# Kernel tuning notes

Measured on AMD Instinct MI355X. Metric: run time of the kernel, lower is better.

## Reference

```python
import math
import jax, jax.numpy as jnp
import numpy as np

B, T, E, H = 8, 2048, 512, 8
NQ_H, NL = 4, 2          # qubits per attention head, circuit layers
NQ_F, FFN = 8, 2048      # FFN qubits, ffn_dim

# ---- batched state-vector quantum simulation -------------------------------
# state shape: [N, 2, 2, ..., 2] (one axis of size 2 per qubit; wire q = axis q+1)

def apply_ry(state, q, theta):
    """RY(theta) on wire q. theta: scalar or [N] (per-batch angle)."""
    th = jnp.asarray(theta) * 0.5
    c, s = jnp.cos(th), jnp.sin(th)
    if th.ndim == 1:
        shp = (-1,) + (1,) * (state.ndim - 2)
        c, s = c.reshape(shp), s.reshape(shp)
    s0 = jax.lax.index_in_dim(state, 0, axis=q + 1, keepdims=False)
    s1 = jax.lax.index_in_dim(state, 1, axis=q + 1, keepdims=False)
    return jnp.stack([c * s0 - s * s1, s * s0 + c * s1], axis=q + 1)

def apply_cnot(state, ctrl, tgt):
    c0 = jax.lax.index_in_dim(state, 0, axis=ctrl + 1, keepdims=True)
    c1 = jax.lax.index_in_dim(state, 1, axis=ctrl + 1, keepdims=True)
    c1 = jnp.flip(c1, axis=tgt + 1)  # X on target when control = 1
    return jnp.concatenate([c0, c1], axis=ctrl + 1)

def run_circuit(x, params):
    """x: [N, n] data angles. params: [L, n] (shared) or [N, L, n] (per-element).
    Circuit: L x (RY(params) layer + CNOT chain + ring CNOT), then RY(x), then <Z_q>.
    Returns [N, n] PauliZ expectations."""
    N, n = x.shape
    L = params.shape[-2]
    state = jnp.zeros((N, 2 ** n), x.dtype).at[:, 0].set(1.0).reshape((N,) + (2,) * n)
    for l in range(L):
        for q in range(n):
            theta = params[:, l, q] if params.ndim == 3 else params[l, q]
            state = apply_ry(state, q, theta)
        for q in range(n - 1):
            state = apply_cnot(state, q, q + 1)
        state = apply_cnot(state, n - 1, 0)
    for q in range(n):
        state = apply_ry(state, q, x[:, q])
    probs = (state ** 2).reshape(N, 2 ** n)
    bits = (jnp.arange(2 ** n)[:, None] >> (n - 1 - jnp.arange(n))) & 1  # wire 0 = MSB
    return probs @ (1 - 2 * bits).astype(x.dtype)  # [N, n]

def layer_norm(x, g, b, eps=1e-5):
    m = x.mean(-1, keepdims=True)
    v = ((x - m) ** 2).mean(-1, keepdims=True)
    return (x - m) / jnp.sqrt(v + eps) * g + b

def setup_inputs() -> dict:
    key = jax.random.key(0)
    ks = jax.random.split(key, 9)
    def lin(k, o, i):
        return jax.random.normal(k, (o, i), jnp.float32) / np.sqrt(i).astype(np.float32)
    return {
        "x": jax.random.normal(ks[0], (B, T, E), jnp.float32),
        "wq": lin(ks[1], E, E), "wk": lin(ks[2], E, E),
        "wv": lin(ks[3], E, E), "wo": lin(ks[4], E, E),
        "head_params": jax.random.normal(ks[5], (H, NL, NQ_H), jnp.float32),
        "ffn_params": jax.random.normal(ks[6], (2, NQ_F), jnp.float32),
        "w1": lin(ks[7], FFN, NQ_F), "w2": lin(ks[8], E, FFN),
        "g1": jnp.ones((E,), jnp.float32), "b1": jnp.zeros((E,), jnp.float32),
        "g2": jnp.ones((E,), jnp.float32), "b2": jnp.zeros((E,), jnp.float32),
    }

def reference(x, wq, wk, wv, wo, head_params, ffn_params, w1, w2, g1, b1, g2, b2):
    Bb, Tt, Ee = x.shape
    hd = Ee // H
    BT = Bb * Tt
    # ---- quantum multi-head attention (dropout = eval/identity) ----
    q = x @ wq.T; k = x @ wk.T; v = x @ wv.T
    scores = jnp.einsum('bte,bse->bts', q, k) / math.sqrt(Ee)  # NOTE: scale by sqrt(E)
    attn = jax.nn.softmax(scores, axis=-1)
    out = jnp.einsum('bts,bse->bte', attn, v)                  # [B,T,E]
    oh = out.reshape(Bb, Tt, H, hd)
    # fold heads into the batch dim; per-head params broadcast per element
    xh = oh[..., :NQ_H].transpose(2, 0, 1, 3).reshape(H * BT, NQ_H)
    ph = jnp.broadcast_to(head_params[:, None], (H, BT, NL, NQ_H)).reshape(H * BT, NL, NQ_H)
    qout = run_circuit(xh, ph)                                  # [H*BT, NQ_H]
    qout = jnp.pad(qout, ((0, 0), (0, hd - NQ_H)))              # zero-pad to head_dim
    qout = qout.reshape(H, Bb, Tt, hd).transpose(1, 2, 0, 3).reshape(Bb, Tt, Ee)
    attn_out = qout @ wo.T
    x1 = layer_norm(x + attn_out, g1, b1)
    # ---- quantum FFN (only ffn_params[0] used, as in source) ----
    xf = x1.reshape(BT, Ee)[:, :NQ_F]
    f = run_circuit(xf, ffn_params[:1]).reshape(Bb, Tt, NQ_F)
    f = jax.nn.relu(f @ w1.T) @ w2.T
    return layer_norm(x1 + f, g2, b2)
```

## Files before the change

kernel.cpp:

```cpp
#include <hip/hip_runtime.h>
#include <hip/hip_bf16.h>
#include <math.h>


#define B_   8
#define T_   2048
#define E_   512

typedef __attribute__((ext_vector_type(8))) short bf16x8;
typedef __attribute__((ext_vector_type(4))) short bf16x4;
typedef __attribute__((ext_vector_type(4))) float f32x4;

#define GLL16(g, l) __builtin_amdgcn_global_load_lds((const __attribute__((address_space(1))) void*)(g), (__attribute__((address_space(3))) void*)(l), 16, 0, 0)

__device__ inline unsigned short f2bf(float f){
  union { float f; unsigned u; } v; v.f = f;
  unsigned r = v.u + 0x7fff + ((v.u >> 16) & 1);
  return (unsigned short)(r >> 16);
}

__global__ __launch_bounds__(256) void k0_setup(const float* __restrict__ hp,
                         const float* __restrict__ fp,
                         const float* __restrict__ wo, float* __restrict__ cAB,
                         unsigned short* __restrict__ wo32b) {
  int t = threadIdx.x, bi = blockIdx.x;
  if (bi > 0) {
    int gid = (bi-1)*256 + t;
    int e = gid >> 3, c4 = gid & 7;
    float4 v = *(const float4*)(wo + (size_t)e*512 + c4*64);
    unsigned short h[4] = { f2bf(v.x), f2bf(v.y), f2bf(v.z), f2bf(v.w) };
    *(unsigned long long*)(wo32b + (size_t)e*32 + c4*4) = *(unsigned long long*)h;
    return;
  }
  __shared__ float fst[256], tmp[256], ra[256], rb[256];
  fst[t] = (t == 0) ? 1.f : 0.f;
  __syncthreads();
  #pragma unroll
  for (int q = 0; q < 8; ++q) {
    int str = 1 << (7-q);
    float th = 0.5f * fp[q];
    float c = cosf(th), s = sinf(th);
    float self = fst[t], part = fst[t ^ str];
    float nv = (t & str) ? (c*self + s*part) : (c*self - s*part);
    __syncthreads();
    tmp[t] = nv;
    __syncthreads();
    fst[t] = tmp[t];
    __syncthreads();
  }
  #pragma unroll
  for (int g = 0; g < 8; ++g) {
    int ctrl = (g < 7) ? g : 7, tgt = (g < 7) ? g+1 : 0;
    int cs = 1 << (7-ctrl), tsr = 1 << (7-tgt);
    float nv = fst[(t & cs) ? (t ^ tsr) : t];
    __syncthreads();
    fst[t] = nv;
    __syncthreads();
  }
  #pragma unroll
  for (int q = 0; q < 8; ++q) {
    int str = 1 << (7-q);
    float a = fst[t]*fst[t] * ((t & str) ? -1.f : 1.f);
    float b = fst[t]*fst[t ^ str];
    ra[t] = a; rb[t] = b;
    __syncthreads();
    for (int off = 128; off > 0; off >>= 1){
      if (t < off){ ra[t] += ra[t+off]; rb[t] += rb[t+off]; }
      __syncthreads();
    }
    if (t == 0){ cAB[64+q] = ra[0]; cAB[72+q] = rb[0]; }
    __syncthreads();
  }
  if (t < 8) {
    float st[16];
    #pragma unroll
    for (int i=0;i<16;i++) st[i]=0.f;
    st[0]=1.f;
    for (int l=0;l<2;l++){
      for (int q=0;q<4;q++){
        float th = 0.5f*hp[t*8 + l*4 + q];
        float c = cosf(th), s = sinf(th);
        int str = 1<<(3-q);
        for (int i=0;i<16;i++) if (!(i & str)) {
          float s0=st[i], s1=st[i|str];
          st[i]     = c*s0 - s*s1;
          st[i|str] = s*s0 + c*s1;
        }
      }
      for (int q=0;q<4;q++){
        int ctrl = (q<3)? q : 3, tgt = (q<3)? q+1 : 0;
        int cs = 1<<(3-ctrl), tsr = 1<<(3-tgt);
        for (int i=0;i<16;i++) if ((i&cs) && !(i&tsr)) {
          float tt = st[i]; st[i]=st[i|tsr]; st[i|tsr]=tt;
        }
      }
    }
    for (int q=0;q<4;q++){
      int str = 1<<(3-q);
      float A=0.f, Bv=0.f;
      for (int i=0;i<16;i++){
        A  += st[i]*st[i] * ((i&str)? -1.f : 1.f);
        Bv += st[i]*st[i^str];
      }
      cAB[t*4+q]    = A;
      cAB[32+t*4+q] = Bv;
    }
  }
}

__global__ __launch_bounds__(256) void kc_cast(const float* __restrict__ x,
                     const float* __restrict__ wq, const float* __restrict__ wk,
                     const float* __restrict__ w2, unsigned short* __restrict__ xb,
                     unsigned short* __restrict__ wqkb, unsigned short* __restrict__ w2b){
  int bi = blockIdx.x;
  if (bi < 4096) {
    int i = bi*256 + threadIdx.x;
    const float4* p = (const float4*)x + (size_t)i*2;
    float4 a = p[0], b = p[1];
    union { unsigned short h[8]; uint4 u; } o;
    o.h[0]=f2bf(a.x); o.h[1]=f2bf(a.y); o.h[2]=f2bf(a.z); o.h[3]=f2bf(a.w);
    o.h[4]=f2bf(b.x); o.h[5]=f2bf(b.y); o.h[6]=f2bf(b.z); o.h[7]=f2bf(b.w);
    ((uint4*)xb)[i] = o.u;
    return;
  }
  int i = (bi-4096)*256 + threadIdx.x;
  const float* src; unsigned short* dst; float s = 1.f;
  if (i < 65536){
    int row = i >> 6, c8 = (i & 63)*8;
    if (row < 512){ src = wq + (size_t)row*512 + c8; s = 0.044194173824159216f; }
    else          { src = wk + (size_t)(row-512)*512 + c8; }
    dst = wqkb + (size_t)row*512 + c8;
  } else {
    int j = i - 65536;
    src = w2 + (size_t)j*8; dst = w2b + (size_t)j*8;
  }
  float4 a = *(const float4*)src, b = *(const float4*)(src+4);
  union { unsigned short h[8]; uint4 u; } o;
  o.h[0]=f2bf(a.x*s); o.h[1]=f2bf(a.y*s); o.h[2]=f2bf(a.z*s); o.h[3]=f2bf(a.w*s);
  o.h[4]=f2bf(b.x*s); o.h[5]=f2bf(b.y*s); o.h[6]=f2bf(b.z*s); o.h[7]=f2bf(b.w*s);
  *(uint4*)dst = o.u;
}

template<int K, int LDC, bool OUTBF, int GX, int GM>
__global__ __launch_bounds__(256,2) void gemm_bt(
    const unsigned short* __restrict__ A, const unsigned short* __restrict__ Bw,
    void* __restrict__ C, int m_base){
  __shared__ __align__(16) char sm[16384];
  char* As = sm; char* Bs = sm + 8192;
  int t = threadIdx.x, w = t>>6, l = t&63;
  int lr = l&15, quad = l>>4;
  int lin = blockIdx.x;
  int n0 = ((lin >> 3) % GX) * 128;
  int m0 = ((lin & 7) * (GM/8) + lin / (8*GX)) * 128;
  int wr = (w>>1)*64, wc = (w&1)*64;
  f32x4 acc[4][4] = {};
  for (int k0 = 0; k0 < K; k0 += 32){
    __syncthreads();
    #pragma unroll
    for (int c = 0; c < 2; ++c){
      int ch = c*256 + t, row = ch>>2, sw = ch&3, lc = sw ^ ((row>>1)&3);
      GLL16(A  + (size_t)(m0+row)*K + k0 + lc*8, As + c*4096 + w*1024);
      GLL16(Bw + (size_t)(n0+row)*K + k0 + lc*8, Bs + c*4096 + w*1024);
    }
    __syncthreads();
    bf16x8 af[4], bg[4];
    #pragma unroll
    for (int i=0;i<4;++i){
      int ra = wr + i*16 + lr;
      af[i] = *(const bf16x8*)(As + ra*64 + (quad ^ ((ra>>1)&3))*16);
      int rb = wc + i*16 + lr;
      bg[i] = *(const bf16x8*)(Bs + rb*64 + (quad ^ ((rb>>1)&3))*16);
    }
    #pragma unroll
    for (int i=0;i<4;++i)
      #pragma unroll
      for (int j=0;j<4;++j)
        acc[i][j] = __builtin_amdgcn_mfma_f32_16x16x32_bf16(af[i], bg[j], acc[i][j], 0,0,0);
  }
  #pragma unroll
  for (int i=0;i<4;++i)
    #pragma unroll
    for (int j=0;j<4;++j)
      #pragma unroll
      for (int r=0;r<4;++r){
        size_t row = (size_t)(m_base + m0 + wr + i*16 + quad*4 + r);
        int col = n0 + wc + j*16 + lr;
        if constexpr (OUTBF) ((unsigned short*)C)[row*LDC + col] = f2bf(acc[i][j][r]);
        else                 ((float*)C)[row*LDC + col] = acc[i][j][r];
      }
}

__global__ __launch_bounds__(256) void k1_v32(const float* __restrict__ x,
    const float* __restrict__ wv, unsigned short* __restrict__ v32t) {
  int m0 = blockIdx.x * 64;
  __shared__ float Xs[64][36];
  __shared__ float Ws[32][36];
  int t = threadIdx.x;
  int m = t >> 2, c0 = (t & 3) * 8;
  float acc[8] = {};
  for (int k0 = 0; k0 < 512; k0 += 32) {
    #pragma unroll
    for (int u=0; u<2; u++){
      int idx = t + u*256;
      int r = idx >> 3, c4 = (idx & 7) * 4;
      *(float4*)&Xs[r][c4] = *(const float4*)(x + (size_t)(m0+r)*512 + k0 + c4);
    }
    { int r = t >> 3, c4 = (t & 7) * 4;
      int wrow = (r>>2)*64 + (r&3);
      *(float4*)&Ws[r][c4] = *(const float4*)(wv + (size_t)wrow*512 + k0 + c4);
    }
    __syncthreads();
    #pragma unroll
    for (int kk=0; kk<32; kk++){
      float xv = Xs[m][kk];
      #pragma unroll
      for (int j=0;j<8;j++) acc[j] += xv * Ws[c0+j][kk];
    }
    __syncthreads();
  }
  int tok = m0 + m, bb = tok >> 11, s = tok & 2047;
  #pragma unroll
  for (int j=0;j<8;j++)
    v32t[((size_t)(bb*32 + c0 + j))*2048 + s] = f2bf(acc[j]);
}

__global__ __launch_bounds__(256,1) void k2_attn(
    const unsigned short* __restrict__ qkb, const unsigned short* __restrict__ v32t,
    float* __restrict__ Opart, float* __restrict__ mlb){
  __shared__ __align__(16) char sm[57856];
  char* Qc  = sm;
  char* Ks  = sm + 8192;
  char* Vts = sm + 40960;
  float* OtL = (float*)sm;
  float* mL  = (float*)(sm + 36864);
  float* lL  = (float*)(sm + 37888);

  int t = threadIdx.x, w = t>>6, l = t&63;
  int lr = l & 15, quad = l >> 4;
  int lin = blockIdx.x;
  int b = lin & 7;
  int m0 = ((lin >> 3) & 31) * 64;
  int half = lin >> 8;
  size_t bT = (size_t)b*2048;
  const char* qbase = (const char*)qkb + (bT + m0)*2048;
  const char* vbase = (const char*)v32t + (size_t)b*32*4096;

  f32x4 Ot[2][4] = {};
  float mold[4] = {-1e30f,-1e30f,-1e30f,-1e30f};
  float lsum[4] = {0.f,0.f,0.f,0.f};

  for (int step = half*4; step < half*4 + 4; ++step){
    int s0 = step*256;
    const char* kbase = (const char*)qkb + (bT + s0)*2048 + 1024;
    __syncthreads();
    {
      int j = t>>3, seg = t&7;
      const uint4* vs = (const uint4*)(vbase + (size_t)j*4096 + (s0 + seg*32)*2);
      uint4* vd = (uint4*)(Vts + j*528 + seg*64);
      vd[0]=vs[0]; vd[1]=vs[1]; vd[2]=vs[2]; vd[3]=vs[3];
    }
    f32x4 acc[4][4] = {};
    for (int ec = 0; ec < 8; ++ec){
      __syncthreads();
      { int row = t>>2, sw = t&3, lc = sw ^ ((row>>1)&3);
        GLL16(qbase + (size_t)row*2048 + ec*128 +      lc*16, Qc +        w*1024);
        GLL16(qbase + (size_t)row*2048 + ec*128 + 64 + lc*16, Qc + 4096 + w*1024);
      }
      #pragma unroll
      for (int rd = 0; rd < 4; ++rd){
        int ch = rd*256 + t, row = ch>>2, sw = ch&3, lc = sw ^ ((row>>1)&3);
        GLL16(kbase + (size_t)row*2048 + ec*128 +      lc*16, Ks +         rd*4096 + w*1024);
        GLL16(kbase + (size_t)row*2048 + ec*128 + 64 + lc*16, Ks + 16384 + rd*4096 + w*1024);
      }
      __syncthreads();
      #pragma unroll
      for (int kk = 0; kk < 2; ++kk){
        bf16x8 af[4], bq[4];
        #pragma unroll
        for (int si = 0; si < 4; ++si){
          int row = w*64 + si*16 + lr;
          af[si] = *(const bf16x8*)(Ks + kk*16384 + row*64 + (quad ^ ((row>>1)&3))*16);
        }
        #pragma unroll
        for (int qj = 0; qj < 4; ++qj){
          int row = qj*16 + lr;
          bq[qj] = *(const bf16x8*)(Qc + kk*4096 + row*64 + (quad ^ ((row>>1)&3))*16);
        }
        #pragma unroll
        for (int si = 0; si < 4; ++si)
          #pragma unroll
          for (int qj = 0; qj < 4; ++qj)
            acc[si][qj] = __builtin_amdgcn_mfma_f32_16x16x32_bf16(af[si], bq[qj], acc[si][qj], 0,0,0);
      }
    }
    bf16x4 aV[2][4];
    #pragma unroll
    for (int vt=0; vt<2; ++vt)
      #pragma unroll
      for (int si=0; si<4; ++si)
        aV[vt][si] = *(const bf16x4*)(Vts + (vt*16+lr)*528 + (w*64 + si*16 + quad*4)*2);
    #pragma unroll
    for (int qj=0; qj<4; ++qj){
      float mt = -1e30f;
      #pragma unroll
      for (int si=0; si<4; ++si)
        #pragma unroll
        for (int r=0;r<4;++r) mt = fmaxf(mt, acc[si][qj][r]);
      mt = fmaxf(mt, __shfl_xor(mt, 16));
      mt = fmaxf(mt, __shfl_xor(mt, 32));
      float mn = fmaxf(mold[qj], mt);
      float al = __expf(mold[qj] - mn);
      mold[qj] = mn;
      float rs = 0.f;
      #pragma unroll
      for (int si=0; si<4; ++si)
        #pragma unroll
        for (int r=0;r<4;++r){
          float p = __expf(acc[si][qj][r] - mn);
          acc[si][qj][r] = p; rs += p;
        }
      rs += __shfl_xor(rs, 16); rs += __shfl_xor(rs, 32);
      lsum[qj] = lsum[qj]*al + rs;
      Ot[0][qj] *= al; Ot[1][qj] *= al;
      #pragma unroll
      for (int si=0; si<4; ++si){
        bf16x4 pb;
        pb[0]=(short)f2bf(acc[si][qj][0]); pb[1]=(short)f2bf(acc[si][qj][1]);
        pb[2]=(short)f2bf(acc[si][qj][2]); pb[3]=(short)f2bf(acc[si][qj][3]);
        Ot[0][qj] = __builtin_amdgcn_mfma_f32_16x16x16bf16_1k(aV[0][si], pb, Ot[0][qj], 0,0,0);
        Ot[1][qj] = __builtin_amdgcn_mfma_f32_16x16x16bf16_1k(aV[1][si], pb, Ot[1][qj], 0,0,0);
      }
    }
  }
  __syncthreads();
  #pragma unroll
  for (int qj=0; qj<4; ++qj){
    if (quad == 0){ mL[w*64 + qj*16 + lr] = mold[qj]; lL[w*64 + qj*16 + lr] = lsum[qj]; }
    *(f32x4*)(OtL + (size_t)(w*64 + qj*16 + lr)*36 + quad*4)      = Ot[0][qj];
    *(f32x4*)(OtL + (size_t)(w*64 + qj*16 + lr)*36 + 16 + quad*4) = Ot[1][qj];
  }
  __syncthreads();
  {
    int qr = t>>2, vg = (t&3)*8;
    float M = -1e30f;
    #pragma unroll
    for (int w4=0; w4<4; ++w4) M = fmaxf(M, mL[w4*64+qr]);
    float L = 0.f; float o[8] = {};
    #pragma unroll
    for (int w4=0; w4<4; ++w4){
      float a = __expf(mL[w4*64+qr] - M);
      L += a * lL[w4*64+qr];
      const float* Op = OtL + (size_t)(w4*64+qr)*36 + vg;
      #pragma unroll
      for (int j=0;j<8;++j) o[j] += a*Op[j];
    }
    size_t tok = bT + m0 + qr;
    float* od = Opart + ((size_t)half*16384 + tok)*32 + vg;
    *(float4*)od     = make_float4(o[0],o[1],o[2],o[3]);
    *(float4*)(od+4) = make_float4(o[4],o[5],o[6],o[7]);
    if ((t&3) == 0){
      mlb[((size_t)half*16384 + tok)*2]     = M;
      mlb[((size_t)half*16384 + tok)*2 + 1] = L;
    }
  }
}

__global__ __launch_bounds__(256) void k2_merge(const float* __restrict__ Opart,
    const float* __restrict__ mlb, const float* __restrict__ cAB,
    unsigned short* __restrict__ q32b){
  int g = blockIdx.x*256 + threadIdx.x;
  int tok = g >> 2, vg = (g & 3) * 8;
  float m0v = mlb[(size_t)tok*2],           l0 = mlb[(size_t)tok*2 + 1];
  float m1v = mlb[(size_t)(16384+tok)*2],   l1 = mlb[(size_t)(16384+tok)*2 + 1];
  float M = fmaxf(m0v, m1v);
  float a0 = __expf(m0v - M), a1 = __expf(m1v - M);
  float inv = 1.f / (a0*l0 + a1*l1);
  const float* O0 = Opart + (size_t)tok*32 + vg;
  const float* O1 = Opart + (size_t)(16384+tok)*32 + vg;
  union { unsigned short h[8]; uint4 u; } res;
  #pragma unroll
  for (int j=0;j<8;++j){
    float ov = (a0*O0[j] + a1*O1[j]) * inv;
    int cc = vg + j;
    res.h[j] = f2bf(cosf(ov)*cAB[cc] - sinf(ov)*cAB[32+cc]);
  }
  *(uint4*)(q32b + (size_t)tok*32 + vg) = res.u;
}

__global__ __launch_bounds__(256) void k3_proj_ln(const float* __restrict__ x,
    const unsigned short* __restrict__ q32b, const unsigned short* __restrict__ wo32b,
    const float* __restrict__ g1, const float* __restrict__ b1,
    const float* __restrict__ cAB, float* __restrict__ x1, float* __restrict__ fbuf) {
  __shared__ __align__(16) char sm3[36224];
  char* Ws = sm3;
  char* Qs = sm3 + 32768;
  float* red1 = (float*)(sm3 + 34816);
  float* red2 = (float*)(sm3 + 35328);
  float* mm   = (float*)(sm3 + 35840);
  float* rr   = (float*)(sm3 + 35968);
  int t = threadIdx.x, w = t>>6, l = t&63, lr = l&15, quad = l>>4;
  int tok0 = blockIdx.x * 32;
  #pragma unroll
  for (int i=0;i<8;++i){
    int g = t + i*256, row = g>>2, ch = g&3;
    uint4 v = ((const uint4*)wo32b)[g];
    *(uint4*)(Ws + row*64 + (ch ^ ((row>>1)&3))*16) = v;
  }
  if (t < 128){
    int row = t>>2, ch = t&3;
    uint4 v = ((const uint4*)(q32b + (size_t)tok0*32))[t];
    *(uint4*)(Qs + row*64 + (ch ^ ((row>>1)&3))*16) = v;
  }
  __syncthreads();
  bf16x8 af[2], bf[8];
  #pragma unroll
  for (int i=0;i<2;++i){
    int m = i*16 + lr;
    af[i] = *(const bf16x8*)(Qs + m*64 + (quad ^ ((m>>1)&3))*16);
  }
  #pragma unroll
  for (int j=0;j<8;++j){
    int n = w*128 + j*16 + lr;
    bf[j] = *(const bf16x8*)(Ws + n*64 + (quad ^ ((n>>1)&3))*16);
  }
  f32x4 acc[2][8];
  #pragma unroll
  for (int i=0;i<2;++i)
    #pragma unroll
    for (int j=0;j<8;++j){
      f32x4 z = {0.f,0.f,0.f,0.f};
      acc[i][j] = __builtin_amdgcn_mfma_f32_16x16x32_bf16(af[i], bf[j], z, 0,0,0);
    }
  float s1[2][4] = {}, s2[2][4] = {};
  #pragma unroll
  for (int i=0;i<2;++i)
    #pragma unroll
    for (int r=0;r<4;++r){
      int m = i*16 + quad*4 + r;
      const float* xrow = x + (size_t)(tok0+m)*512 + w*128 + lr;
      #pragma unroll
      for (int j=0;j<8;++j){
        float v = acc[i][j][r] + xrow[j*16];
        acc[i][j][r] = v;
        s1[i][r] += v; s2[i][r] += v*v;
      }
    }
  #pragma unroll
  for (int off=1; off<16; off<<=1){
    #pragma unroll
    for (int i=0;i<2;++i)
      #pragma unroll
      for (int r=0;r<4;++r){
        s1[i][r] += __shfl_xor(s1[i][r], off);
        s2[i][r] += __shfl_xor(s2[i][r], off);
      }
  }
  if (lr == 0){
    #pragma unroll
    for (int i=0;i<2;++i)
      #pragma unroll
      for (int r=0;r<4;++r){
        int m = i*16 + quad*4 + r;
        red1[w*32 + m] = s1[i][r];
        red2[w*32 + m] = s2[i][r];
      }
  }
  __syncthreads();
  if (t < 32){
    float a = red1[t] + red1[32+t] + red1[64+t] + red1[96+t];
    float bb = red2[t] + red2[32+t] + red2[64+t] + red2[96+t];
    float mean = a * (1.f/512.f);
    float var  = bb * (1.f/512.f) - mean*mean;
    mm[t] = mean; rr[t] = rsqrtf(var + 1e-5f);
  }
  __syncthreads();
  float g1v[8], b1v[8];
  #pragma unroll
  for (int j=0;j<8;++j){
    int n = w*128 + j*16 + lr;
    g1v[j] = g1[n]; b1v[j] = b1[n];
  }
  #pragma unroll
  for (int i=0;i<2;++i)
    #pragma unroll
    for (int r=0;r<4;++r){
      int m = i*16 + quad*4 + r;
      float mean = mm[m], rstd = rr[m];
      float* orow = x1 + (size_t)(tok0+m)*512 + w*128 + lr;
      #pragma unroll
      for (int j=0;j<8;++j){
        float nv = (acc[i][j][r]-mean)*rstd*g1v[j] + b1v[j];
        orow[j*16] = nv;
        if (w == 0 && j == 0 && lr < 8)
          fbuf[(size_t)(tok0+m)*8 + lr] = cosf(nv)*cAB[64+lr] - sinf(nv)*cAB[72+lr];
      }
    }
}

__global__ __launch_bounds__(256,2) void k4_ffn(
    const float* __restrict__ fbuf, const float* __restrict__ w1,
    const unsigned short* __restrict__ w2b, float* __restrict__ C){
  __shared__ __align__(16) char sm4[19456];
  char* As = sm4; char* Bs = sm4 + 8192;
  float* w1s = (float*)(sm4 + 16384);
  int t = threadIdx.x, w = t>>6, l = t&63;
  int lr = l&15, quad = l>>4;
  int lin = blockIdx.x;
  int n0 = ((lin >> 3) & 3) * 128;
  int m0 = ((lin & 7) * 16 + (lin >> 5)) * 128;
  int wr = (w>>1)*64, wc = (w&1)*64;
  int rg = t & 31, cg = t >> 5;
  float f[4][8];
  #pragma unroll
  for (int j=0;j<4;++j){
    const float4* fp4 = (const float4*)(fbuf + (size_t)(m0 + rg*4 + j)*8);
    float4 a = fp4[0], b = fp4[1];
    f[j][0]=a.x; f[j][1]=a.y; f[j][2]=a.z; f[j][3]=a.w;
    f[j][4]=b.x; f[j][5]=b.y; f[j][6]=b.z; f[j][7]=b.w;
  }
  if (t < 64){
    int row = t>>1, hf = t&1;
    float4 v = *(const float4*)(w1 + row*8 + hf*4);
    *(float4*)(w1s + row*12 + hf*4) = v;
  }
  f32x4 acc[4][4] = {};
  __syncthreads();
  for (int s = 0; s < 64; ++s){
    int k0 = s*32;
    const float* wcur = w1s + (s&1)*384;
    float*       wnxt = w1s + ((s+1)&1)*384;
    #pragma unroll
    for (int c = 0; c < 2; ++c){
      int ch = c*256 + t, row = ch>>2, sw = ch&3, lc = sw ^ ((row>>1)&3);
      GLL16(w2b + (size_t)(n0+row)*2048 + k0 + lc*8, Bs + c*4096 + w*1024);
    }
    float4 vn = {0.f,0.f,0.f,0.f};
    if (t < 64 && s < 63){
      int row = t>>1, hf = t&1;
      vn = *(const float4*)(w1 + (size_t)(k0 + 32 + row)*8 + hf*4);
    }
    float wv[4][8];
    #pragma unroll
    for (int j=0;j<4;++j){
      const float* wp = wcur + (cg*4 + j)*12;
      float4 a = *(const float4*)wp, b = *(const float4*)(wp + 4);
      wv[j][0]=a.x; wv[j][1]=a.y; wv[j][2]=a.z; wv[j][3]=a.w;
      wv[j][4]=b.x; wv[j][5]=b.y; wv[j][6]=b.z; wv[j][7]=b.w;
    }
    #pragma unroll
    for (int i=0;i<4;++i){
      bf16x4 hb;
      #pragma unroll
      for (int j=0;j<4;++j){
        float sa = f[i][0]*wv[j][0];
        #pragma unroll
        for (int c=1;c<8;++c) sa += f[i][c]*wv[j][c];
        hb[j] = (short)f2bf(fmaxf(sa, 0.f));
      }
      int m = rg*4 + i;
      *(bf16x4*)(As + m*64 + (((cg>>1) ^ ((m>>1)&3))<<4) + ((cg&1)<<3)) = hb;
    }
    if (t < 64 && s < 63){
      int row = t>>1, hf = t&1;
      *(float4*)(wnxt + row*12 + hf*4) = vn;
    }
    __syncthreads();
    bf16x8 af[4], bg[4];
    #pragma unroll
    for (int i=0;i<4;++i){
      int ra = wr + i*16 + lr;
      af[i] = *(const bf16x8*)(As + ra*64 + (quad ^ ((ra>>1)&3))*16);
      int rb = wc + i*16 + lr;
      bg[i] = *(const bf16x8*)(Bs + rb*64 + (quad ^ ((rb>>1)&3))*16);
    }
    #pragma unroll
    for (int i=0;i<4;++i)
      #pragma unroll
      for (int j=0;j<4;++j)
        acc[i][j] = __builtin_amdgcn_mfma_f32_16x16x32_bf16(af[i], bg[j], acc[i][j], 0,0,0);
    __syncthreads();
  }
  #pragma unroll
  for (int i=0;i<4;++i)
    #pragma unroll
    for (int j=0;j<4;++j)
      #pragma unroll
      for (int r=0;r<4;++r){
        size_t row = (size_t)(m0 + wr + i*16 + quad*4 + r);
        int col = n0 + wc + j*16 + lr;
        C[row*512 + col] = acc[i][j][r];
      }
}

__global__ __launch_bounds__(256) void k5_ln2(const float* __restrict__ x1,
    const float* __restrict__ g2, const float* __restrict__ b2,
    float* __restrict__ out) {
  int tok = blockIdx.x, t = threadIdx.x;
  __shared__ float rs1[4], rs2[4], mv[2];
  float vals[2], ssum=0.f, ssq=0.f;
  #pragma unroll
  for (int u=0;u<2;u++){
    int e = t + u*256;
    float s = x1[(size_t)tok*512 + e] + out[(size_t)tok*512 + e];
    vals[u]=s; ssum+=s; ssq+=s*s;
  }
  #pragma unroll
  for (int off=32; off>0; off>>=1){ ssum += __shfl_down(ssum,off); ssq += __shfl_down(ssq,off); }
  int wid = t >> 6;
  if ((t & 63) == 0){ rs1[wid]=ssum; rs2[wid]=ssq; }
  __syncthreads();
  if (t == 0){
    float a = rs1[0]+rs1[1]+rs1[2]+rs1[3];
    float b = rs2[0]+rs2[1]+rs2[2]+rs2[3];
    float mean = a * (1.f/512.f);
    float var  = b * (1.f/512.f) - mean*mean;
    mv[0]=mean; mv[1]=rsqrtf(var + 1e-5f);
  }
  __syncthreads();
  float mean=mv[0], rstd=mv[1];
  #pragma unroll
  for (int u=0;u<2;u++){
    int e = t + u*256;
    out[(size_t)tok*512 + e] = (vals[u]-mean)*rstd*g2[e] + b2[e];
  }
}

extern "C" void kernel_launch(void* const* d_in, const int* in_sizes, int n_in,
                              void* d_out, int out_size, void* d_ws, size_t ws_size,
                              hipStream_t stream) {
  const float* x  = (const float*)d_in[0];
  const float* wq = (const float*)d_in[1];
  const float* wk = (const float*)d_in[2];
  const float* wv = (const float*)d_in[3];
  const float* wo = (const float*)d_in[4];
  const float* hp = (const float*)d_in[5];
  const float* fp = (const float*)d_in[6];
  const float* w1 = (const float*)d_in[7];
  const float* w2 = (const float*)d_in[8];
  const float* g1 = (const float*)d_in[9];
  const float* b1 = (const float*)d_in[10];
  const float* g2 = (const float*)d_in[11];
  const float* b2 = (const float*)d_in[12];
  float* out = (float*)d_out;
  float* ws  = (float*)d_ws;

  unsigned short* qkb  = (unsigned short*)(ws);
  float*          x1   = ws + 8388608;
  unsigned short* xb   = (unsigned short*)(ws + 16777216);
  unsigned short* wqkb = (unsigned short*)(ws + 20971520);
  unsigned short* w2b  = (unsigned short*)(ws + 21233664);
  unsigned short* v32t = (unsigned short*)(ws + 21757952);
  unsigned short* q32b = (unsigned short*)(ws + 22020096);
  float*          fbuf = ws + 22544384;
  unsigned short* wo32b= (unsigned short*)(ws + 22675456);
  float*          cAB  = ws + 22691840;
  float*          Opart= ws + 22691968;
  float*          mlb  = ws + 23740544;

  k0_setup<<<17, 256, 0, stream>>>(hp, fp, wo, cAB, wo32b);
  kc_cast<<<4864, 256, 0, stream>>>(x, wq, wk, w2, xb, wqkb, w2b);
  gemm_bt<512,1024,true,8,128><<<1024, 256, 0, stream>>>(xb, wqkb, qkb, 0);
  k1_v32<<<256, 256, 0, stream>>>(x, wv, v32t);
  k2_attn<<<512, 256, 0, stream>>>(qkb, v32t, Opart, mlb);
  k2_merge<<<256, 256, 0, stream>>>(Opart, mlb, cAB, q32b);
  k3_proj_ln<<<512, 256, 0, stream>>>(x, q32b, wo32b, g1, b1, cAB, x1, fbuf);
  k4_ffn<<<512, 256, 0, stream>>>(fbuf, w1, w2b, out);
  k5_ln2<<<16384, 256, 0, stream>>>(x1, g2, b2, out);
}
```

Before: 417.3 us.

## Retile FFN kernel to 64-row blocks spanning all 512 output columns

The fused FFN kernel used 128x128 output tiles, so each block recomputed relu(f@w1^T) for its 128 rows across four column tiles. It now uses 512-thread blocks that own 64 rows and all 512 output columns, so the hidden activations are computed once per row instead of four times. The w1 tile in shared memory also gets padding to reduce bank conflicts. In exchange, each block stages the full 512-row w2 slice per k-step, which needs much more LDS, and the grid halves to 256 blocks, which lowers occupancy.

```diff
diff --git a/kernel.cpp b/kernel.cpp
--- a/kernel.cpp
+++ b/kernel.cpp
@@ -497,80 +497,64 @@
     }
 }
 
-__global__ __launch_bounds__(256,2) void k4_ffn(
+__global__ __launch_bounds__(512,2) void k4_ffn(
     const float* __restrict__ fbuf, const float* __restrict__ w1,
     const unsigned short* __restrict__ w2b, float* __restrict__ C){
-  __shared__ __align__(16) char sm4[19456];
-  char* As = sm4; char* Bs = sm4 + 8192;
-  float* w1s = (float*)(sm4 + 16384);
+  __shared__ __align__(16) char sm4[40192];
+  char* As = sm4;
+  char* Bs = sm4 + 4096;
+  float* w1s = (float*)(sm4 + 36864);
   int t = threadIdx.x, w = t>>6, l = t&63;
   int lr = l&15, quad = l>>4;
-  int lin = blockIdx.x;
-  int n0 = ((lin >> 3) & 3) * 128;
-  int m0 = ((lin & 7) * 16 + (lin >> 5)) * 128;
-  int wr = (w>>1)*64, wc = (w&1)*64;
-  int rg = t & 31, cg = t >> 5;
-  float f[4][8];
-  #pragma unroll
-  for (int j=0;j<4;++j){
-    const float4* fp4 = (const float4*)(fbuf + (size_t)(m0 + rg*4 + j)*8);
-    float4 a = fp4[0], b = fp4[1];
-    f[j][0]=a.x; f[j][1]=a.y; f[j][2]=a.z; f[j][3]=a.w;
-    f[j][4]=b.x; f[j][5]=b.y; f[j][6]=b.z; f[j][7]=b.w;
-  }
+  int m0 = blockIdx.x * 64;
+  int am = t>>3, cg = t&7;
+  const float4* fp4 = (const float4*)(fbuf + (size_t)(m0 + am)*8);
+  float4 fa = fp4[0], fb = fp4[1];
   if (t < 64){
     int row = t>>1, hf = t&1;
     float4 v = *(const float4*)(w1 + row*8 + hf*4);
-    *(float4*)(w1s + row*12 + hf*4) = v;
+    *(float4*)(w1s + row*12 + (row>>2)*4 + hf*4) = v;
   }
   f32x4 acc[4][4] = {};
   __syncthreads();
   for (int s = 0; s < 64; ++s){
     int k0 = s*32;
-    const float* wcur = w1s + (s&1)*384;
-    float*       wnxt = w1s + ((s+1)&1)*384;
-    #pragma unroll
-    for (int c = 0; c < 2; ++c){
-      int ch = c*256 + t, row = ch>>2, sw = ch&3, lc = sw ^ ((row>>1)&3);
-      GLL16(w2b + (size_t)(n0+row)*2048 + k0 + lc*8, Bs + c*4096 + w*1024);
+    const float* wcur = w1s + (s&1)*416;
+    float*       wnxt = w1s + ((s+1)&1)*416;
+    #pragma unroll
+    for (int c = 0; c < 4; ++c){
+      int ch = c*512 + t, row = ch>>2, sw = ch&3, lc = sw ^ ((row>>1)&3);
+      GLL16(w2b + (size_t)row*2048 + k0 + lc*8, Bs + c*8192 + w*1024);
     }
     float4 vn = {0.f,0.f,0.f,0.f};
     if (t < 64 && s < 63){
       int row = t>>1, hf = t&1;
       vn = *(const float4*)(w1 + (size_t)(k0 + 32 + row)*8 + hf*4);
     }
-    float wv[4][8];
-    #pragma unroll
-    for (int j=0;j<4;++j){
-      const float* wp = wcur + (cg*4 + j)*12;
-      float4 a = *(const float4*)wp, b = *(const float4*)(wp + 4);
-      wv[j][0]=a.x; wv[j][1]=a.y; wv[j][2]=a.z; wv[j][3]=a.w;
-      wv[j][4]=b.x; wv[j][5]=b.y; wv[j][6]=b.z; wv[j][7]=b.w;
-    }
-    #pragma unroll
-    for (int i=0;i<4;++i){
+    {
       bf16x4 hb;
+      const float* wp = wcur + cg*52;
       #pragma unroll
       for (int j=0;j<4;++j){
-        float sa = f[i][0]*wv[j][0];
-        #pragma unroll
-        for (int c=1;c<8;++c) sa += f[i][c]*wv[j][c];
+        float4 wa = *(const float4*)(wp + j*12);
+        float4 wb = *(const float4*)(wp + j*12 + 4);
+        float sa = fa.x*wa.x + fa.y*wa.y + fa.z*wa.z + fa.w*wa.w
+                 + fb.x*wb.x + fb.y*wb.y + fb.z*wb.z + fb.w*wb.w;
         hb[j] = (short)f2bf(fmaxf(sa, 0.f));
       }
-      int m = rg*4 + i;
-      *(bf16x4*)(As + m*64 + (((cg>>1) ^ ((m>>1)&3))<<4) + ((cg&1)<<3)) = hb;
+      *(bf16x4*)(As + am*64 + (((cg>>1) ^ ((am>>1)&3))<<4) + ((cg&1)<<3)) = hb;
     }
     if (t < 64 && s < 63){
       int row = t>>1, hf = t&1;
-      *(float4*)(wnxt + row*12 + hf*4) = vn;
+      *(float4*)(wnxt + row*12 + (row>>2)*4 + hf*4) = vn;
     }
     __syncthreads();
     bf16x8 af[4], bg[4];
     #pragma unroll
     for (int i=0;i<4;++i){
-      int ra = wr + i*16 + lr;
+      int ra = i*16 + lr;
       af[i] = *(const bf16x8*)(As + ra*64 + (quad ^ ((ra>>1)&3))*16);
-      int rb = wc + i*16 + lr;
+      int rb = w*64 + i*16 + lr;
       bg[i] = *(const bf16x8*)(Bs + rb*64 + (quad ^ ((rb>>1)&3))*16);
     }
     #pragma unroll
@@ -586,8 +570,8 @@
     for (int j=0;j<4;++j)
       #pragma unroll
       for (int r=0;r<4;++r){
-        size_t row = (size_t)(m0 + wr + i*16 + quad*4 + r);
-        int col = n0 + wc + j*16 + lr;
+        size_t row = (size_t)(m0 + i*16 + quad*4 + r);
+        int col = w*64 + j*16 + lr;
         C[row*512 + col] = acc[i][j][r];
       }
 }
@@ -664,6 +648,6 @@
   k2_attn<<<512, 256, 0, stream>>>(qkb, v32t, Opart, mlb);
   k2_merge<<<256, 256, 0, stream>>>(Opart, mlb, cAB, q32b);
   k3_proj_ln<<<512, 256, 0, stream>>>(x, q32b, wo32b, g1, b1, cAB, x1, fbuf);
-  k4_ffn<<<512, 256, 0, stream>>>(fbuf, w1, w2b, out);
+  k4_ffn<<<256, 512, 0, stream>>>(fbuf, w1, w2b, out);
   k5_ln2<<<16384, 256, 0, stream>>>(x1, g2, b2, out);
 }
```

Result: faster. 408.5 us (-2.1%).
